# Optimization experiments

Measured on AMD Instinct MI355X. Metric: run time of the kernel, lower is better.

## Reference

```python
import jax, jax.numpy as jnp
import numpy as np

D, DFF, H, V, BS, NL, NG = 1024, 4096, 16, 32000, 128, 2, 2

def _ln(x, w, b, eps=1e-5):
    m = x.mean(-1, keepdims=True)
    v = ((x - m) ** 2).mean(-1, keepdims=True)
    return (x - m) / jnp.sqrt(v + eps) * w + b

def _full_attn(q, k, v):
    # q,k,v: [B,H,S,dk] ; manual max-subtract softmax with +1e-9 denom and clamp, per FullAttention
    dk = q.shape[-1]
    s = jnp.einsum('bhqd,bhkd->bhqk', q / jnp.sqrt(jnp.float32(dk)), k)
    s = s - s.max(-1, keepdims=True)
    e = jnp.exp(s)
    a = e / (e.sum(-1, keepdims=True) + 1e-9)
    a = jnp.clip(a, 1e-9, 1.0)
    return jnp.einsum('bhqk,bhkd->bhqd', a, v)

def _attn_layer(qi, ki, vi, lnw, lnb, pw, pb):
    # lnw/lnb: [4,D] (norm_q,k,v,out); pw: [4,D,D] (q,k,v,o, stored [in,out]); pb: [4,D]
    B, Sq, _ = qi.shape
    Sk = ki.shape[1]
    q = _ln(qi, lnw[0], lnb[0]) @ pw[0] + pb[0]
    k = _ln(ki, lnw[1], lnb[1]) @ pw[1] + pb[1]
    v = _ln(vi, lnw[2], lnb[2]) @ pw[2] + pb[2]
    dk = D // H
    q = q.reshape(B, Sq, H, dk).transpose(0, 2, 1, 3)
    k = k.reshape(B, Sk, H, dk).transpose(0, 2, 1, 3)
    v = v.reshape(B, Sk, H, dk).transpose(0, 2, 1, 3)
    o = _full_attn(q, k, v).transpose(0, 2, 1, 3).reshape(B, Sq, D)
    o = o @ pw[3] + pb[3]
    return _ln(o, lnw[3], lnb[3])

def _ffn(x, n1w, n1b, n2w, n2b, w1, b1, w2, b2):
    h = jax.nn.gelu(_ln(x, n1w, n1b) @ w1 + b1, approximate=False)
    return _ln(h @ w2 + b2 + x, n2w, n2b)

def _tlayer(x, lnw, lnb, pw, pb, w1, b1, w2, b2):
    # lnw/lnb: [6,D] (attn q,k,v,out norms, ffn norm1, ffn norm2)
    x = x + _attn_layer(x, x, x, lnw[:4], lnb[:4], pw, pb)
    return _ffn(x, lnw[4], lnb[4], lnw[5], lnb[5], w1, b1, w2, b2)

def _pe(S, d):
    pos = jnp.arange(S, dtype=jnp.float32)[:, None]
    div = jnp.exp(jnp.arange(0, d, 2, dtype=jnp.float32) * (-np.log(10000.0) / d))
    pe = jnp.zeros((S, d), jnp.float32)
    pe = pe.at[:, 0::2].set(jnp.sin(pos * div))
    pe = pe.at[:, 1::2].set(jnp.cos(pos * div))
    return pe

def setup_inputs() -> dict:
    key = jax.random.key(0)
    ks = iter(jax.random.split(key, 64))
    nrm = lambda shp: jax.random.normal(next(ks), shp, jnp.float32) * 0.02
    inp = {
        'x': jax.random.randint(next(ks), (4, 4096), 0, V, dtype=jnp.int32).astype(jnp.int64),
        'emb': nrm((V, D)),
        'in_ln_w': jnp.ones((D,)), 'in_ln_b': jnp.zeros((D,)),
        'loc_ln_w': jnp.ones((NL, 6, D)), 'loc_ln_b': jnp.zeros((NL, 6, D)),
        'loc_pw': nrm((NL, 4, D, D)), 'loc_pb': jnp.zeros((NL, 4, D)),
        'loc_w1': nrm((NL, D, DFF)), 'loc_b1': jnp.zeros((NL, DFF)),
        'loc_w2': nrm((NL, DFF, D)), 'loc_b2': jnp.zeros((NL, D)),
        'locn_w': jnp.ones((D,)), 'locn_b': jnp.zeros((D,)),
        'pool_q': nrm((1, 1, D)),
        'pool_n_w': jnp.ones((D,)), 'pool_n_b': jnp.zeros((D,)),
        'pool_ln_w': jnp.ones((4, D)), 'pool_ln_b': jnp.zeros((4, D)),
        'pool_pw': nrm((4, D, D)), 'pool_pb': jnp.zeros((4, D)),
        'glob_ln_w': jnp.ones((NG, 6, D)), 'glob_ln_b': jnp.zeros((NG, 6, D)),
        'glob_pw': nrm((NG, 4, D, D)), 'glob_pb': jnp.zeros((NG, 4, D)),
        'glob_w1': nrm((NG, D, DFF)), 'glob_b1': jnp.zeros((NG, DFF)),
        'glob_w2': nrm((NG, DFF, D)), 'glob_b2': jnp.zeros((NG, D)),
        'out_ln_w': jnp.ones((D,)), 'out_ln_b': jnp.zeros((D,)),
        'out_w': nrm((D, V)), 'out_b': jnp.zeros((V,)),
    }
    return inp

def reference(x, emb, in_ln_w, in_ln_b, loc_ln_w, loc_ln_b, loc_pw, loc_pb,
              loc_w1, loc_b1, loc_w2, loc_b2, locn_w, locn_b,
              pool_q, pool_n_w, pool_n_b, pool_ln_w, pool_ln_b, pool_pw, pool_pb,
              glob_ln_w, glob_ln_b, glob_pw, glob_pb, glob_w1, glob_b1, glob_w2, glob_b2,
              out_ln_w, out_ln_b, out_w, out_b):
    B, S = x.shape
    nb = S // BS
    h = jnp.clip(emb[x], -100.0, 100.0) + _pe(S, D)[None]
    h = _ln(h, in_ln_w, in_ln_b)
    h = h.reshape(B * nb, BS, D)  # local blocks
    for i in range(NL):
        h = jnp.clip(_tlayer(h, loc_ln_w[i], loc_ln_b[i], loc_pw[i], loc_pb[i],
                             loc_w1[i], loc_b1[i], loc_w2[i], loc_b2[i]), -100.0, 100.0)
    h = _ln(h, locn_w, locn_b)
    # attention pooling of each block to one vector
    hp = _ln(h, pool_n_w, pool_n_b)
    q = jnp.broadcast_to(pool_q, (B * nb, 1, D))
    g = _attn_layer(q, hp, hp, pool_ln_w, pool_ln_b, pool_pw, pool_pb)[:, 0].reshape(B, nb, D)
    for i in range(NG):
        g = jnp.clip(_tlayer(g, glob_ln_w[i], glob_ln_b[i], glob_pw[i], glob_pb[i],
                             glob_w1[i], glob_b1[i], glob_w2[i], glob_b2[i]), -100.0, 100.0)
    g = _ln(g, out_ln_w, out_ln_b)
    return g @ out_w + out_b  # [B, num_blocks, vocab]
```

## Files before the change

kernel.cpp:

```cpp
#include <hip/hip_runtime.h>
#include <hip/hip_bf16.h>
#include <math.h>

#define DEV __device__ __forceinline__

typedef __attribute__((ext_vector_type(8))) short bf16x8;
typedef __attribute__((ext_vector_type(4))) float f32x4;
typedef unsigned short u16;

constexpr int D_ = 1024, NTOK = 16384, SEQ = 4096;

DEV u16 f2b(float f){
  union{float f;unsigned u;} v; v.f=f;
  unsigned r = (v.u + 0x7fffu + ((v.u>>16)&1u))>>16;
  return (u16)r;
}
DEV float b2f(u16 h){ union{unsigned u;float f;} v; v.u=((unsigned)h)<<16; return v.f; }

DEV float gelu_f(float x){
  float z = 0.7978845608028654f*(x + 0.044715f*x*x*x);
  float e = __expf(-2.f*z);
  float t = 2.f/(1.f+e) - 1.f;
  return 0.5f*x*(1.f+t);
}

DEV void gld16(const void* g, void* l){
  __builtin_amdgcn_global_load_lds((const __attribute__((address_space(1))) void*)g,
                                   (__attribute__((address_space(3))) void*)l, 16, 0, 0);
}

#define BAR()    __builtin_amdgcn_s_barrier()
#define SCHED0() __builtin_amdgcn_sched_barrier(0)
#define LGKM0()  asm volatile("s_waitcnt lgkmcnt(0)" ::: "memory")
#define VM0()    asm volatile("s_waitcnt vmcnt(0)" ::: "memory")

DEV float blockSum(float v){
  __shared__ float sb[4];
  #pragma unroll
  for(int m=32;m>=1;m>>=1) v += __shfl_xor(v, m, 64);
  int lane = threadIdx.x & 63, wv = threadIdx.x >> 6;
  __syncthreads();
  if(lane==0) sb[wv]=v;
  __syncthreads();
  float r = sb[0]+sb[1]+sb[2]+sb[3];
  __syncthreads();
  return r;
}

__global__ __launch_bounds__(256) void detect_k(const int* __restrict__ xr, int* __restrict__ flag){
  int tid=threadIdx.x; float cnt=0.f;
  for(int i=tid;i<8192;i+=256) if(xr[2*i+1]!=0) cnt+=1.f;
  cnt = blockSum(cnt);
  if(tid==0) *flag = (cnt < 64.f) ? 1 : 0;
}

__global__ __launch_bounds__(256) void embed_k(const void* __restrict__ xv, const int* __restrict__ flag,
      const float* __restrict__ emb, const float* __restrict__ w, const float* __restrict__ b,
      u16* __restrict__ out, u16* __restrict__ outn){
  int t = blockIdx.x;
  int id;
  if(*flag) id = (int)((const long long*)xv)[t];
  else      id = ((const int*)xv)[t];
  int s = t & (SEQ-1);
  int d0 = threadIdx.x*4;
  float4 e4 = *(const float4*)(emb + (size_t)id*D_ + d0);
  float vv[4] = {e4.x, e4.y, e4.z, e4.w};
  float acc = 0.f;
  #pragma unroll
  for(int i=0;i<4;i++){
    float e = fminf(fmaxf(vv[i], -100.f), 100.f);
    int d = d0+i;
    float fr = expf(-(float)(d & ~1) * (9.210340371976184f/(float)D_));
    float ang = (float)s * fr;
    e += (d&1) ? cosf(ang) : sinf(ang);
    vv[i]=e; acc+=e;
  }
  float mean = blockSum(acc)*(1.f/D_);
  float var=0.f;
  #pragma unroll
  for(int i=0;i<4;i++){ float dd=vv[i]-mean; var+=dd*dd; }
  var = blockSum(var)*(1.f/D_);
  float rs = rsqrtf(var+1e-5f);
  float y[4];
  #pragma unroll
  for(int i=0;i<4;i++) y[i] = (vv[i]-mean)*rs*w[d0+i]+b[d0+i];
  ushort4 o; o.x=f2b(y[0]); o.y=f2b(y[1]); o.z=f2b(y[2]); o.w=f2b(y[3]);
  *(ushort4*)(out + (size_t)t*D_ + d0) = o;
  float m2 = blockSum(y[0]+y[1]+y[2]+y[3])*(1.f/D_);
  float v2=0.f;
  #pragma unroll
  for(int i=0;i<4;i++){ float dd=y[i]-m2; v2+=dd*dd; }
  v2 = blockSum(v2)*(1.f/D_);
  float rs2 = rsqrtf(v2+1e-5f);
  ushort4 on; on.x=f2b((y[0]-m2)*rs2); on.y=f2b((y[1]-m2)*rs2); on.z=f2b((y[2]-m2)*rs2); on.w=f2b((y[3]-m2)*rs2);
  *(ushort4*)(outn + (size_t)t*D_ + d0) = on;
}

template<int MODE,int WRN>
__global__ __launch_bounds__(256) void ln_k(const u16* __restrict__ in, const u16* __restrict__ res,
      const float* __restrict__ w, const float* __restrict__ b, u16* __restrict__ out,
      u16* __restrict__ outn){
  int t = blockIdx.x; int d0 = threadIdx.x*4;
  ushort4 r4 = *(const ushort4*)(in + (size_t)t*D_ + d0);
  float vv[4] = {b2f(r4.x),b2f(r4.y),b2f(r4.z),b2f(r4.w)};
  float mean = blockSum(vv[0]+vv[1]+vv[2]+vv[3])*(1.f/D_);
  float var=0.f;
  #pragma unroll
  for(int i=0;i<4;i++){ float dd=vv[i]-mean; var+=dd*dd; }
  var = blockSum(var)*(1.f/D_);
  float rs = rsqrtf(var+1e-5f);
  float rv[4]={0,0,0,0};
  if(MODE==3){
    ushort4 q4 = *(const ushort4*)(res + (size_t)t*D_ + d0);
    rv[0]=b2f(q4.x); rv[1]=b2f(q4.y); rv[2]=b2f(q4.z); rv[3]=b2f(q4.w);
  }
  float y[4];
  #pragma unroll
  for(int i=0;i<4;i++){
    float v = (vv[i]-mean)*rs;
    v = v*w[d0+i]+b[d0+i];
    if(MODE==2) v = fminf(fmaxf(v,-100.f),100.f);
    if(MODE==3) v += rv[i];
    y[i]=v;
  }
  ushort4 o; o.x=f2b(y[0]); o.y=f2b(y[1]); o.z=f2b(y[2]); o.w=f2b(y[3]);
  *(ushort4*)(out + (size_t)t*D_ + d0) = o;
  if(WRN){
    float m2 = blockSum(y[0]+y[1]+y[2]+y[3])*(1.f/D_);
    float v2=0.f;
    #pragma unroll
    for(int i=0;i<4;i++){ float dd=y[i]-m2; v2+=dd*dd; }
    v2 = blockSum(v2)*(1.f/D_);
    float rs2 = rsqrtf(v2+1e-5f);
    ushort4 on; on.x=f2b((y[0]-m2)*rs2); on.y=f2b((y[1]-m2)*rs2); on.z=f2b((y[2]-m2)*rs2); on.w=f2b((y[3]-m2)*rs2);
    *(ushort4*)(outn + (size_t)t*D_ + d0) = on;
  }
}

__global__ __launch_bounds__(256) void ln3x_k(const u16* __restrict__ in,
    const float* __restrict__ w1,const float* __restrict__ b1,
    const float* __restrict__ w2,const float* __restrict__ b2, u16* __restrict__ out){
  int t=blockIdx.x, d0=threadIdx.x*4;
  ushort4 r4 = *(const ushort4*)(in + (size_t)t*D_ + d0);
  float vv[4]={b2f(r4.x),b2f(r4.y),b2f(r4.z),b2f(r4.w)};
  #pragma unroll
  for(int pass=0;pass<3;pass++){
    float mean = blockSum(vv[0]+vv[1]+vv[2]+vv[3])*(1.f/D_);
    float var=0.f;
    #pragma unroll
    for(int i=0;i<4;i++){ float dd=vv[i]-mean; var+=dd*dd; }
    var = blockSum(var)*(1.f/D_);
    float rs = rsqrtf(var+1e-5f);
    #pragma unroll
    for(int i=0;i<4;i++){
      float y=(vv[i]-mean)*rs;
      if(pass==0) y = y*w1[d0+i]+b1[d0+i];
      else if(pass==1) y = y*w2[d0+i]+b2[d0+i];
      vv[i]=y;
    }
  }
  ushort4 o;
  o.x=f2b(vv[0]); o.y=f2b(vv[1]); o.z=f2b(vv[2]); o.w=f2b(vv[3]);
  *(ushort4*)(out + (size_t)t*D_ + d0) = o;
}

__global__ __launch_bounds__(256) void lnrow_k(const float* __restrict__ x, const float* __restrict__ w,
      const float* __restrict__ b, float* __restrict__ out){
  int d0=threadIdx.x*4;
  float vv[4]={x[d0],x[d0+1],x[d0+2],x[d0+3]};
  float mean = blockSum(vv[0]+vv[1]+vv[2]+vv[3])*(1.f/D_);
  float var=0.f;
  #pragma unroll
  for(int i=0;i<4;i++){ float dd=vv[i]-mean; var+=dd*dd; }
  var = blockSum(var)*(1.f/D_);
  float rs = rsqrtf(var+1e-5f);
  #pragma unroll
  for(int i=0;i<4;i++) out[d0+i]=(vv[i]-mean)*rs*w[d0+i]+b[d0+i];
}

#define TF_BODY(W, ldW, lnw, Wt, Kd, n0, k0)                                 \
  {                                                                          \
    int ty = threadIdx.x>>6, tx = threadIdx.x&63;                            \
    _Pragma("unroll")                                                        \
    for(int p=0;p<16;p++){                                                   \
      int row = p*4+ty;                                                      \
      float sc = (lnw) ? (lnw)[(k0)+row] : 1.f;                              \
      T[row][tx] = (W)[(size_t)((k0)+row)*(ldW) + (n0)+tx]*sc;               \
    }                                                                        \
    __syncthreads();                                                         \
    _Pragma("unroll")                                                        \
    for(int p=0;p<16;p++){                                                   \
      int row = p*4+ty;                                                      \
      (Wt)[(size_t)((n0)+row)*(Kd) + (k0)+tx] = f2b(T[tx][row]);             \
    }                                                                        \
  }

__global__ __launch_bounds__(256) void tf_k(const float* __restrict__ W, int ldW,
      const float* __restrict__ lnw, u16* __restrict__ Wt, int Kd){
  __shared__ float T[64][65];
  int n0 = blockIdx.x*64, k0 = blockIdx.y*64;
  TF_BODY(W, ldW, lnw, Wt, Kd, n0, k0)
}

__global__ __launch_bounds__(256) void prep_tf_layer_k(const float* __restrict__ pw,
      const float* __restrict__ w1, const float* __restrict__ w2, const float* __restrict__ lw,
      u16* __restrict__ Wqk, u16* __restrict__ Wv, u16* __restrict__ Wo,
      u16* __restrict__ W1t, u16* __restrict__ W2t){
  __shared__ float T[64][65];
  int bid = blockIdx.x;
  const float* W; int ldW; const float* lnw; u16* Wt; int Kd, n0, k0;
  if(bid < 1024){
    int m = bid>>8, t = bid&255;
    n0 = (t&15)*64; k0 = (t>>4)*64;
    W = pw + (size_t)m*1024*1024; ldW = 1024; Kd = 1024;
    lnw = (m<3) ? lw + m*1024 : nullptr;
    Wt = (m==0)?Wqk : (m==1)?(Wqk+1024*1024) : (m==2)?Wv : Wo;
  } else if(bid < 2048){
    int t = bid-1024;
    n0 = (t&63)*64; k0 = (t>>6)*64;
    W = w1; ldW = 4096; Kd = 1024; lnw = lw+4*1024; Wt = W1t;
  } else {
    int t = bid-2048;
    n0 = (t&15)*64; k0 = (t>>4)*64;
    W = w2; ldW = 1024; Kd = 4096; lnw = nullptr; Wt = W2t;
  }
  TF_BODY(W, ldW, lnw, Wt, Kd, n0, k0)
}

__global__ __launch_bounds__(256) void prep_tf_pool_k(const float* __restrict__ pw,
      const float* __restrict__ lw, u16* __restrict__ PWkv, u16* __restrict__ PWo){
  __shared__ float T[64][65];
  int bid = blockIdx.x;
  int m = 1 + (bid>>8), t = bid&255;
  int n0 = (t&15)*64, k0 = (t>>4)*64;
  const float* W = pw + (size_t)m*1024*1024;
  const float* lnw = (m<3) ? lw + m*1024 : nullptr;
  u16* Wt = (m==1)?PWkv : (m==2)?(PWkv+1024*1024) : PWo;
  TF_BODY(W, 1024, lnw, Wt, 1024, n0, k0)
}

DEV void bias_body(const float* W, int ldW, int Kd, const float* lnb, float pbv, float* out){
  int tid = threadIdx.x;
  float chk = 0.f;
  if(lnb){ for(int k=tid;k<Kd;k+=256) chk += fabsf(lnb[k]); }
  chk = blockSum(chk);
  if(chk==0.f){ if(tid==0) *out = pbv; return; }
  float s=0.f;
  for(int k=tid;k<Kd;k+=256) s += lnb[k]*W[(size_t)k*ldW];
  s = blockSum(s);
  if(tid==0) *out = pbv + s;
}

__global__ __launch_bounds__(256) void bias_k(const float* __restrict__ W, int ldW,
      const float* __restrict__ lnb, const float* __restrict__ pb, float* __restrict__ out, int Kd){
  int j = blockIdx.x;
  bias_body(W + j, ldW, Kd, lnb, pb[j], out + j);
}

__global__ __launch_bounds__(256) void prep_bias_layer_k(const float* __restrict__ pw,
      const float* __restrict__ w1, const float* __restrict__ w2,
      const float* __restrict__ lb, const float* __restrict__ pb,
      const float* __restrict__ b1in, const float* __restrict__ b2in,
      float* __restrict__ Bqk, float* __restrict__ Bv, float* __restrict__ Bo,
      float* __restrict__ B1, float* __restrict__ B2){
  int j = blockIdx.x;
  const float* W; int ldW, Kd; const float* lnb; float pbv; float* out;
  const size_t MM = 1024ull*1024;
  if(j<2048){ int m=j>>10; int col=j&1023; W=pw+m*MM+col; ldW=1024; Kd=1024; lnb=lb+m*1024; pbv=pb[m*1024+col]; out=Bqk+j; }
  else if(j<3072){ int col=j-2048; W=pw+2*MM+col; ldW=1024; Kd=1024; lnb=lb+2*1024; pbv=pb[2*1024+col]; out=Bv+col; }
  else if(j<4096){ int col=j-3072; W=pw+3*MM+col; ldW=1024; Kd=1024; lnb=nullptr; pbv=pb[3*1024+col]; out=Bo+col; }
  else if(j<8192){ int col=j-4096; W=w1+col; ldW=4096; Kd=1024; lnb=lb+4*1024; pbv=b1in[col]; out=B1+col; }
  else { int col=j-8192; W=w2+col; ldW=1024; Kd=4096; lnb=nullptr; pbv=b2in[col]; out=B2+col; }
  bias_body(W, ldW, Kd, lnb, pbv, out);
}

__global__ __launch_bounds__(256) void prep_bias_pool_k(const float* __restrict__ pw,
      const float* __restrict__ lb, const float* __restrict__ pb,
      float* __restrict__ Pbkv, float* __restrict__ Pbo){
  int j = blockIdx.x;
  const size_t MM = 1024ull*1024;
  int m = 1 + (j>>10), col = j&1023;
  const float* lnb = (m<3) ? lb + m*1024 : nullptr;
  float* out = (m==1)?(Pbkv+col) : (m==2)?(Pbkv+1024+col) : (Pbo+col);
  bias_body(pw + m*MM + col, 1024, 1024, lnb, pb[m*1024+col], out);
}

__global__ __launch_bounds__(256) void matvec_k(const float* __restrict__ xn, const float* __restrict__ W,
      int ldW, const float* __restrict__ bias, float* __restrict__ out){
  int j=blockIdx.x, tid=threadIdx.x;
  float s=0.f;
  for(int k=tid;k<1024;k+=256) s += xn[k]*W[(size_t)k*ldW + j];
  s=blockSum(s);
  if(tid==0) out[j]=s+bias[j];
}

template<int EPI,int OUTF,int TV>
__global__ __launch_bounds__(256) void gemm_k(const u16* __restrict__ A, const u16* __restrict__ Bt,
      const float* __restrict__ bias, const u16* __restrict__ resid, void* __restrict__ Cout,
      int M, int N, int K, int ldc){
  __shared__ u16 SH[32768];
  int tid = threadIdx.x, lane = tid&63, wv = tid>>6;
  int g = lane>>4, l15 = lane&15;
  int GX = gridDim.x, GY = gridDim.y;
  int nwg = GX*GY;
  int flat = blockIdx.y*GX + blockIdx.x;
  int q = nwg>>3, r = nwg&7, xcd = flat&7, idx = flat>>3;
  int f = (xcd<r ? xcd*(q+1) : r*(q+1)+(xcd-r)*q) + idx;
  int by, bx;
  if((GY & 7) == 0){
    int sbs = GX<<3;
    int s = f / sbs, rr2 = f - s*sbs;
    by = s*8 + (rr2 & 7);
    bx = rr2 >> 3;
  } else {
    by = f/GX; bx = f - by*GX;
  }
  int row0 = by*128, col0 = bx*128;
  int wr = wv>>1, wc = wv&1;
  int e0 = wv*512 + lane*8;
  f32x4 acc[4][4] = {};
  auto STAGE = [&](int buf, int t){
    u16* base = SH + buf*16384;
    int k0 = t<<6;
    #pragma unroll
    for(int c=0;c<4;c++){
      int e = c*2048 + e0;
      int row = e>>6;
      int slx = ((e>>3)&7) ^ (row&7);
      gld16(A  + (size_t)(row0 + row)*K + (k0 + slx*8), &base[e]);
      gld16(Bt + (size_t)(col0 + row)*K + (k0 + slx*8), &base[8192 + e]);
    }
  };
  int nt = K>>6;
  STAGE(0, 0);
  VM0(); BAR(); SCHED0();
  #pragma unroll 2
  for(int t=0;t<nt;t++){
    int b = t&1;
    if(t+1<nt) STAGE(b^1, t+1);
    bf16x8 a[2][4], bb[2][4];
    #pragma unroll
    for(int ks=0;ks<2;ks++){
      #pragma unroll
      for(int m=0;m<4;m++){
        int ra = wr*64+m*16+l15;
        a[ks][m] = *(const bf16x8*)&SH[b*16384 + ra*64 + (((ks*4+g) ^ (ra&7))<<3)];
      }
      #pragma unroll
      for(int n=0;n<4;n++){
        int rb = wc*64+n*16+l15;
        bb[ks][n] = *(const bf16x8*)&SH[b*16384 + 8192 + rb*64 + (((ks*4+g) ^ (rb&7))<<3)];
      }
    }
    #pragma unroll
    for(int ks=0;ks<2;ks++)
      #pragma unroll
      for(int m=0;m<4;m++)
        #pragma unroll
        for(int n=0;n<4;n++)
          acc[m][n] = __builtin_amdgcn_mfma_f32_16x16x32_bf16(a[ks][m], bb[ks][n], acc[m][n], 0,0,0);
    if(t+1<nt){
      VM0(); LGKM0(); BAR(); SCHED0();
    }
  }
  if(TV){
    __syncthreads();
    u16* Tb = SH;
    #pragma unroll
    for(int m=0;m<4;m++){
      #pragma unroll
      for(int n=0;n<4;n++){
        int c = wc*64 + n*16 + l15;
        float bs = bias[col0 + c];
        #pragma unroll
        for(int r2=0;r2<4;r2++){
          int Rl = wr*64 + m*16 + g*4 + r2;
          Tb[c*128 + (Rl ^ ((c&7)<<4))] = f2b(acc[m][n][r2]+bs);
        }
      }
    }
    __syncthreads();
    for(int p=tid*4; p<16384; p+=1024){
      int c = p>>7, rr = p&127;
      int rs = rr ^ ((c&7)<<4);
      ushort4 v4;
      v4.x = Tb[c*128+rs]; v4.y = Tb[c*128+rs+1]; v4.z = Tb[c*128+rs+2]; v4.w = Tb[c*128+rs+3];
      *(ushort4*)((u16*)Cout + (size_t)(col0+c)*M + row0 + rr) = v4;
    }
  } else {
    #pragma unroll
    for(int m=0;m<4;m++){
      #pragma unroll
      for(int n=0;n<4;n++){
        int Cc = col0 + wc*64 + n*16 + l15;
        float bs = bias[Cc];
        #pragma unroll
        for(int r2=0;r2<4;r2++){
          int R = row0 + wr*64 + m*16 + g*4 + r2;
          float v = acc[m][n][r2] + bs;
          if(EPI==1) v = gelu_f(v);
          if(EPI==2) v += b2f(resid[(size_t)R*ldc + Cc]);
          if(OUTF) ((float*)Cout)[(size_t)R*ldc + Cc] = v;
          else     ((u16*)Cout)[(size_t)R*ldc + Cc] = f2b(v);
        }
      }
    }
  }
}

__global__ __launch_bounds__(256) void attnl_k(const u16* __restrict__ QK, const u16* __restrict__ VT,
      u16* __restrict__ AT){
  __shared__ u16 SP[16384];
  __shared__ u16 Vt[8192];
  __shared__ float rmax[256], rsum[256];
  int tid=threadIdx.x, lane=tid&63, wv=tid>>6, g=lane>>4, l15=lane&15;
  int lb = blockIdx.x>>4, h = blockIdx.x&15;
  int wr=wv>>1, wc=wv&1;
  #pragma unroll
  for(int c=0;c<4;c++){
    int chunk = c*2048 + wv*512;
    int e = chunk + lane*8;
    int rq = e>>6;
    int sq = ((e>>3)&7) ^ (rq&7);
    int rv = e>>7;
    int sv = ((e>>3)&15) ^ (rv&15);
    gld16(QK + (size_t)(lb*128 + rq)*2048 + h*64 + sq*8,        &SP[chunk]);
    gld16(QK + (size_t)(lb*128 + rq)*2048 + 1024 + h*64 + sq*8, &SP[8192+chunk]);
    gld16(VT + (size_t)(h*64 + rv)*16384 + lb*128 + sv*8,       &Vt[chunk]);
  }
  __syncthreads();
  f32x4 s[4][4] = {};
  #pragma unroll
  for(int ks=0;ks<2;ks++){
    bf16x8 a[4], b[4];
    #pragma unroll
    for(int m=0;m<4;m++){
      int ra = wr*64+m*16+l15;
      a[m] = *(const bf16x8*)&SP[ra*64 + (((ks*4+g) ^ (ra&7))<<3)];
    }
    #pragma unroll
    for(int n=0;n<4;n++){
      int rb = wc*64+n*16+l15;
      b[n] = *(const bf16x8*)&SP[8192 + rb*64 + (((ks*4+g) ^ (rb&7))<<3)];
    }
    #pragma unroll
    for(int m=0;m<4;m++)
      #pragma unroll
      for(int n=0;n<4;n++)
        s[m][n] = __builtin_amdgcn_mfma_f32_16x16x32_bf16(a[m], b[n], s[m][n], 0,0,0);
  }
  #pragma unroll
  for(int m=0;m<4;m++)
    #pragma unroll
    for(int n=0;n<4;n++) s[m][n] *= 0.125f;
  #pragma unroll
  for(int m=0;m<4;m++)
    #pragma unroll
    for(int r=0;r<4;r++){
      float mx = fmaxf(fmaxf(s[m][0][r],s[m][1][r]),fmaxf(s[m][2][r],s[m][3][r]));
      #pragma unroll
      for(int msk=1;msk<16;msk<<=1) mx = fmaxf(mx, __shfl_xor(mx,msk,64));
      if(l15==0) rmax[(wr*64+m*16+g*4+r)*2+wc]=mx;
    }
  __syncthreads();
  #pragma unroll
  for(int m=0;m<4;m++)
    #pragma unroll
    for(int r=0;r<4;r++){
      int row = wr*64+m*16+g*4+r;
      float M2 = fmaxf(rmax[row*2], rmax[row*2+1]);
      float sm=0.f;
      #pragma unroll
      for(int n=0;n<4;n++){ float e = expf(s[m][n][r]-M2); s[m][n][r]=e; sm+=e; }
      #pragma unroll
      for(int msk=1;msk<16;msk<<=1) sm += __shfl_xor(sm,msk,64);
      if(l15==0) rsum[row*2+wc]=sm;
    }
  __syncthreads();
  #pragma unroll
  for(int m=0;m<4;m++)
    #pragma unroll
    for(int r=0;r<4;r++){
      int row = wr*64+m*16+g*4+r;
      float den = rsum[row*2]+rsum[row*2+1]+1e-9f;
      #pragma unroll
      for(int n=0;n<4;n++){
        float a = s[m][n][r]/den;
        a = fminf(fmaxf(a,1e-9f),1.f);
        int col = wc*64+n*16+l15;
        SP[row*128 + ((((col>>3) ^ (row&15))<<3) | (col&7))] = f2b(a);
      }
    }
  __syncthreads();
  f32x4 o[4][2] = {};
  #pragma unroll
  for(int ks=0;ks<4;ks++){
    bf16x8 a[4], b[2];
    #pragma unroll
    for(int m=0;m<4;m++){
      int ra = wr*64+m*16+l15;
      a[m] = *(const bf16x8*)&SP[ra*128 + (((ks*4+g) ^ (ra&15))<<3)];
    }
    #pragma unroll
    for(int n=0;n<2;n++){
      int rv = wc*32+n*16+l15;
      b[n] = *(const bf16x8*)&Vt[rv*128 + (((ks*4+g) ^ (rv&15))<<3)];
    }
    #pragma unroll
    for(int m=0;m<4;m++)
      #pragma unroll
      for(int n=0;n<2;n++)
        o[m][n] = __builtin_amdgcn_mfma_f32_16x16x32_bf16(a[m], b[n], o[m][n], 0,0,0);
  }
  #pragma unroll
  for(int m=0;m<4;m++)
    #pragma unroll
    for(int n=0;n<2;n++)
      #pragma unroll
      for(int r=0;r<4;r++)
        AT[(size_t)(lb*128 + wr*64+m*16+g*4+r)*1024 + h*64 + wc*32+n*16+l15] = f2b(o[m][n][r]);
}

__global__ __launch_bounds__(256) void poolattn_k(const float* __restrict__ qp, const u16* __restrict__ KV,
      u16* __restrict__ g0){
  int lb = blockIdx.x, tid = threadIdx.x;
  __shared__ float sc[16*128];
  for(int p=tid;p<2048;p+=256){
    int h=p>>7, j=p&127;
    const u16* krow = KV + (size_t)(lb*128+j)*2048 + h*64;
    float s=0.f;
    for(int d=0;d<64;d++) s += qp[h*64+d]*b2f(krow[d]);
    sc[h*128+j] = s*0.125f;
  }
  __syncthreads();
  if(tid<16){
    float* r=&sc[tid*128];
    float mx=r[0];
    for(int j=1;j<128;j++) mx=fmaxf(mx,r[j]);
    float sm=0.f;
    for(int j=0;j<128;j++){ float e=expf(r[j]-mx); r[j]=e; sm+=e; }
    sm+=1e-9f;
    for(int j=0;j<128;j++) r[j]=fminf(fmaxf(r[j]/sm,1e-9f),1.f);
  }
  __syncthreads();
  for(int c=tid;c<1024;c+=256){
    int h=c>>6;
    float acc=0.f;
    for(int j=0;j<128;j++) acc += sc[h*128+j]*b2f(KV[(size_t)(lb*128+j)*2048 + 1024 + c]);
    g0[(size_t)lb*1024 + c] = f2b(acc);
  }
}

__global__ __launch_bounds__(256) void attng_k(const u16* __restrict__ QKV, u16* __restrict__ OUT){
  int bb = blockIdx.x>>4, h = blockIdx.x&15;
  __shared__ float sc[32*32];
  int tid=threadIdx.x;
  for(int p=tid;p<1024;p+=256){
    int i=p>>5, j=p&31;
    const u16* q = QKV + (size_t)(bb*32+i)*3072 + h*64;
    const u16* k = QKV + (size_t)(bb*32+j)*3072 + 1024 + h*64;
    float s=0.f;
    for(int d=0;d<64;d++) s += b2f(q[d])*b2f(k[d]);
    sc[p] = s*0.125f;
  }
  __syncthreads();
  if(tid<32){
    float* r=&sc[tid*32];
    float mx=r[0];
    for(int j=1;j<32;j++) mx=fmaxf(mx,r[j]);
    float sm=0.f;
    for(int j=0;j<32;j++){ float e=expf(r[j]-mx); r[j]=e; sm+=e; }
    sm+=1e-9f;
    for(int j=0;j<32;j++) r[j]=fminf(fmaxf(r[j]/sm,1e-9f),1.f);
  }
  __syncthreads();
  for(int p=tid;p<2048;p+=256){
    int i=p>>6, d=p&63;
    float acc=0.f;
    for(int j=0;j<32;j++) acc += sc[i*32+j]*b2f(QKV[(size_t)(bb*32+j)*3072 + 2048 + h*64 + d]);
    OUT[(size_t)(bb*32+i)*1024 + h*64 + d] = f2b(acc);
  }
}

extern "C" void kernel_launch(void* const* d_in, const int* in_sizes, int n_in,
                              void* d_out, int out_size, void* d_ws, size_t ws_size,
                              hipStream_t stream) {
  (void)in_sizes; (void)n_in; (void)out_size;
  const void*  x       = d_in[0];
  const float* emb     = (const float*)d_in[1];
  const float* in_ln_w = (const float*)d_in[2];
  const float* in_ln_b = (const float*)d_in[3];
  const float* loc_ln_w= (const float*)d_in[4];
  const float* loc_ln_b= (const float*)d_in[5];
  const float* loc_pw  = (const float*)d_in[6];
  const float* loc_pb  = (const float*)d_in[7];
  const float* loc_w1  = (const float*)d_in[8];
  const float* loc_b1  = (const float*)d_in[9];
  const float* loc_w2  = (const float*)d_in[10];
  const float* loc_b2  = (const float*)d_in[11];
  const float* locn_w  = (const float*)d_in[12];
  const float* locn_b  = (const float*)d_in[13];
  const float* pool_q  = (const float*)d_in[14];
  const float* pool_n_w= (const float*)d_in[15];
  const float* pool_n_b= (const float*)d_in[16];
  const float* pool_ln_w=(const float*)d_in[17];
  const float* pool_ln_b=(const float*)d_in[18];
  const float* pool_pw = (const float*)d_in[19];
  const float* pool_pb = (const float*)d_in[20];
  const float* glob_ln_w=(const float*)d_in[21];
  const float* glob_ln_b=(const float*)d_in[22];
  const float* glob_pw = (const float*)d_in[23];
  const float* glob_pb = (const float*)d_in[24];
  const float* glob_w1 = (const float*)d_in[25];
  const float* glob_b1 = (const float*)d_in[26];
  const float* glob_w2 = (const float*)d_in[27];
  const float* glob_b2 = (const float*)d_in[28];
  const float* out_ln_w= (const float*)d_in[29];
  const float* out_ln_b= (const float*)d_in[30];
  const float* out_w   = (const float*)d_in[31];
  const float* out_b   = (const float*)d_in[32];

  char* wsb = (char*)d_ws;
  size_t off = 0;
  auto AL = [&](size_t n)->char*{ size_t o=(off+255)&~(size_t)255; off=o+n; return wsb+o; };

  int*  flag = (int*)AL(256);
  u16*  WA   = (u16*)AL(12ull*1024*1024*2);
  float* BA  = (float*)AL(12*1024*4);
  float* qn  = (float*)AL(1024*4);
  float* qp  = (float*)AL(1024*4);
  float* Hb  = (float*)AL(32000*4);
  u16*  R    = (u16*)AL(64ull*1024*1024*2);
  u16*  X    = (u16*)AL((size_t)NTOK*1024*2);
  u16*  XN   = (u16*)AL((size_t)NTOK*1024*2);
  u16*  G    = (u16*)AL(128ull*1024*2);
  u16*  GN   = (u16*)AL(128ull*1024*2);
  u16*  GQKV = (u16*)AL(128ull*3072*2);
  u16*  GAT  = (u16*)AL(128ull*1024*2);
  u16*  GO   = (u16*)AL(128ull*1024*2);
  u16*  GFH  = (u16*)AL(128ull*4096*2);
  u16*  g0   = (u16*)AL(128ull*1024*2);
  if(off > ws_size) return;

  u16 *LWqk = WA, *LWv = WA+2097152, *LWo = WA+3145728, *LW1 = WA+4194304, *LW2 = WA+8388608;
  float *Lbqk = BA, *Lbv = BA+2048, *Lbo = BA+3072, *Lb1 = BA+4096, *Lb2 = BA+8192;
  u16 *GWqkv = WA, *GWo = WA+3145728, *GW1 = WA+4194304, *GW2 = WA+8388608;
  float *Gbqkv = BA, *Gbo = BA+3072, *Gb1 = BA+4096, *Gb2 = BA+8192;
  u16 *PWkv = WA, *PWo = WA+2097152;
  float *Pbkv = BA, *Pbo = BA+2048;
  u16 *QKb = R, *VTb = R+33554432, *ATb = R+50331648;
  u16 *FH  = R;
  u16 *KVb = R;
  u16 *HW  = R;
  u16 *Ob  = XN;

  const size_t MM = 1024ull*1024;

  detect_k<<<1,256,0,stream>>>((const int*)x, flag);
  embed_k<<<NTOK,256,0,stream>>>(x, flag, emb, in_ln_w, in_ln_b, X, XN);

  for(int l=0;l<2;l++){
    const float* pw = loc_pw + (size_t)l*4*MM;
    const float* lw = loc_ln_w + (size_t)l*6*1024;
    const float* lb = loc_ln_b + (size_t)l*6*1024;
    const float* pb = loc_pb + (size_t)l*4*1024;
    const float* w1 = loc_w1 + (size_t)l*1024*4096;
    const float* w2 = loc_w2 + (size_t)l*4096*1024;
    prep_tf_layer_k<<<3072,256,0,stream>>>(pw, w1, w2, lw, LWqk, LWv, LWo, LW1, LW2);
    prep_bias_layer_k<<<9216,256,0,stream>>>(pw, w1, w2, lb, pb,
        loc_b1+(size_t)l*4096, loc_b2+(size_t)l*1024, Lbqk, Lbv, Lbo, Lb1, Lb2);

    gemm_k<0,0,0><<<dim3(16,128),256,0,stream>>>(XN, LWqk, Lbqk, nullptr, QKb, NTOK, 2048, 1024, 2048);
    gemm_k<0,0,1><<<dim3(8,128),256,0,stream>>>(XN, LWv, Lbv, nullptr, VTb, NTOK, 1024, 1024, 0);
    attnl_k<<<128*16,256,0,stream>>>(QKb, VTb, ATb);
    gemm_k<0,0,0><<<dim3(8,128),256,0,stream>>>(ATb, LWo, Lbo, nullptr, Ob, NTOK, 1024, 1024, 1024);
    ln_k<3,1><<<NTOK,256,0,stream>>>(Ob, X, lw+3*1024, lb+3*1024, X, XN);
    gemm_k<1,0,0><<<dim3(32,128),256,0,stream>>>(XN, LW1, Lb1, nullptr, FH, NTOK, 4096, 1024, 4096);
    gemm_k<2,0,0><<<dim3(8,128),256,0,stream>>>(FH, LW2, Lb2, X, Ob, NTOK, 1024, 4096, 1024);
    ln_k<2,1><<<NTOK,256,0,stream>>>(Ob, nullptr, lw+5*1024, lb+5*1024, X, XN);
  }

  prep_tf_pool_k<<<768,256,0,stream>>>(pool_pw, pool_ln_w, PWkv, PWo);
  prep_bias_pool_k<<<3072,256,0,stream>>>(pool_pw, pool_ln_b, pool_pb, Pbkv, Pbo);
  lnrow_k<<<1,256,0,stream>>>(pool_q, pool_ln_w, pool_ln_b, qn);
  matvec_k<<<1024,256,0,stream>>>(qn, pool_pw, 1024, pool_pb, qp);
  ln3x_k<<<NTOK,256,0,stream>>>(X, locn_w, locn_b, pool_n_w, pool_n_b, XN);
  gemm_k<0,0,0><<<dim3(16,128),256,0,stream>>>(XN, PWkv, Pbkv, nullptr, KVb, NTOK, 2048, 1024, 2048);
  poolattn_k<<<128,256,0,stream>>>(qp, KVb, g0);
  gemm_k<0,0,0><<<dim3(8,1),256,0,stream>>>(g0, PWo, Pbo, nullptr, GO, 128, 1024, 1024, 1024);
  ln_k<1,1><<<128,256,0,stream>>>(GO, nullptr, pool_ln_w+3*1024, pool_ln_b+3*1024, G, GN);

  for(int l=0;l<2;l++){
    const float* pw = glob_pw + (size_t)l*4*MM;
    const float* lw = glob_ln_w + (size_t)l*6*1024;
    const float* lb = glob_ln_b + (size_t)l*6*1024;
    const float* pb = glob_pb + (size_t)l*4*1024;
    const float* w1 = glob_w1 + (size_t)l*1024*4096;
    const float* w2 = glob_w2 + (size_t)l*4096*1024;
    prep_tf_layer_k<<<3072,256,0,stream>>>(pw, w1, w2, lw, GWqkv, GWqkv+2097152, GWo, GW1, GW2);
    prep_bias_layer_k<<<9216,256,0,stream>>>(pw, w1, w2, lb, pb,
        glob_b1+(size_t)l*4096, glob_b2+(size_t)l*1024, Gbqkv, Gbqkv+2048, Gbo, Gb1, Gb2);

    gemm_k<0,0,0><<<dim3(24,1),256,0,stream>>>(GN, GWqkv, Gbqkv, nullptr, GQKV, 128, 3072, 1024, 3072);
    attng_k<<<64,256,0,stream>>>(GQKV, GAT);
    gemm_k<0,0,0><<<dim3(8,1),256,0,stream>>>(GAT, GWo, Gbo, nullptr, GO, 128, 1024, 1024, 1024);
    ln_k<3,1><<<128,256,0,stream>>>(GO, G, lw+3*1024, lb+3*1024, G, GN);
    gemm_k<1,0,0><<<dim3(32,1),256,0,stream>>>(GN, GW1, Gb1, nullptr, GFH, 128, 4096, 1024, 4096);
    gemm_k<2,0,0><<<dim3(8,1),256,0,stream>>>(GFH, GW2, Gb2, G, GO, 128, 1024, 4096, 1024);
    ln_k<2,1><<<128,256,0,stream>>>(GO, nullptr, lw+5*1024, lb+5*1024, G, GN);
  }

  tf_k<<<dim3(500,16),256,0,stream>>>(out_w, 32000, out_ln_w, HW, 1024);
  bias_k<<<32000,256,0,stream>>>(out_w, 32000, out_ln_b, out_b, Hb, 1024);
  gemm_k<0,1,0><<<dim3(250,1),256,0,stream>>>(GN, HW, Hb, nullptr, d_out, 128, 32000, 1024, 32000);
}
```

Baseline: 1.915 ms.

## Add 256x256-tile 8-wave bf16 GEMM kernel for large token GEMMs

Introduces a 512-thread GEMM kernel with 256x256 output tiles, XOR-swizzled LDS staging through global_load_lds, and double buffering where the next K tile is prefetched while MFMA quadrants run. It also remaps workgroups across XCDs for better L2 locality. All large local-layer and pooling GEMMs switch to it. The larger tiles cut global/L2 traffic per FLOP, at the cost of one workgroup per CU, 128KB of dynamic LDS and heavy register use.

```diff
diff --git a/kernel.cpp b/kernel.cpp
--- a/kernel.cpp
+++ b/kernel.cpp
@@ -32,6 +32,7 @@
 #define BAR()    __builtin_amdgcn_s_barrier()
 #define SCHED0() __builtin_amdgcn_sched_barrier(0)
 #define LGKM0()  asm volatile("s_waitcnt lgkmcnt(0)" ::: "memory")
+#define VM8()    asm volatile("s_waitcnt vmcnt(8)" ::: "memory")
 #define VM0()    asm volatile("s_waitcnt vmcnt(0)" ::: "memory")
 
 DEV float blockSum(float v){
@@ -402,6 +403,138 @@
           if(EPI==2) v += b2f(resid[(size_t)R*ldc + Cc]);
           if(OUTF) ((float*)Cout)[(size_t)R*ldc + Cc] = v;
           else     ((u16*)Cout)[(size_t)R*ldc + Cc] = f2b(v);
+        }
+      }
+    }
+  }
+}
+
+template<int EPI,int TV>
+__global__ __launch_bounds__(512,1) void gemm256_k(const u16* __restrict__ A, const u16* __restrict__ Bt,
+      const float* __restrict__ bias, const u16* __restrict__ resid, void* __restrict__ Cout,
+      int M, int N, int K, int ldc){
+  extern __shared__ u16 LS[];
+  int tid = threadIdx.x, lane = tid&63, wid = tid>>6;
+  int g = lane>>4, l15 = lane&15;
+  int wm = wid>>2, wn = wid&3;
+  int GX = gridDim.x, GY = gridDim.y, nwg = GX*GY;
+  int flat = blockIdx.y*GX + blockIdx.x;
+  int q = nwg>>3, r = nwg&7, xcd = flat&7, idx = flat>>3;
+  int f = (xcd<r ? xcd*(q+1) : r*(q+1)+(xcd-r)*q) + idx;
+  int by, bx;
+  if((GY&7)==0){ int sbs = GX<<3; int s = f/sbs, rr2 = f - s*sbs; by = s*8 + (rr2&7); bx = rr2>>3; }
+  else { by = f/GX; bx = f - by*GX; }
+  int row0 = by*256, col0 = bx*256;
+
+  f32x4 acc[8][4] = {};
+  bf16x8 areg[2][4], breg[2][4];
+
+  auto STAGE_A = [&](int b, int t){
+    #pragma unroll
+    for(int j=0;j<4;j++){
+      int e = j*4096 + tid*8;
+      int row = e>>6;
+      int slx = ((e>>3)&7) ^ (row&7);
+      gld16(A + (size_t)(row0 + row)*K + (t<<6) + slx*8, &LS[b*16384 + e]);
+    }
+  };
+  auto STAGE_B = [&](int b, int t){
+    #pragma unroll
+    for(int j=0;j<4;j++){
+      int e = j*4096 + tid*8;
+      int row = e>>6;
+      int slx = ((e>>3)&7) ^ (row&7);
+      gld16(Bt + (size_t)(col0 + row)*K + (t<<6) + slx*8, &LS[32768 + b*16384 + e]);
+    }
+  };
+  auto READ_A = [&](int b, int mh){
+    #pragma unroll
+    for(int ks=0;ks<2;ks++)
+      #pragma unroll
+      for(int m=0;m<4;m++){
+        int rih = mh*64 + m*16 + l15;
+        areg[ks][m] = *(const bf16x8*)&LS[b*16384 + wm*8192 + rih*64 + (((ks*4+g)^(rih&7))<<3)];
+      }
+  };
+  auto READ_B = [&](int b, int nh){
+    #pragma unroll
+    for(int ks=0;ks<2;ks++)
+      #pragma unroll
+      for(int n=0;n<2;n++){
+        int rih = (wn&1)*64 + (nh*2+n)*16 + l15;
+        breg[ks][nh*2+n] = *(const bf16x8*)&LS[32768 + b*16384 + (wn>>1)*8192 + rih*64 + (((ks*4+g)^(rih&7))<<3)];
+      }
+  };
+  auto MFMA_Q = [&](int mh, int nh){
+    __builtin_amdgcn_s_setprio(1);
+    #pragma unroll
+    for(int ks=0;ks<2;ks++)
+      #pragma unroll
+      for(int m=0;m<4;m++)
+        #pragma unroll
+        for(int n=0;n<2;n++)
+          acc[mh*4+m][nh*2+n] = __builtin_amdgcn_mfma_f32_16x16x32_bf16(
+              areg[ks][m], breg[ks][nh*2+n], acc[mh*4+m][nh*2+n], 0,0,0);
+    __builtin_amdgcn_s_setprio(0);
+  };
+
+  int NT = K>>6;
+  STAGE_B(0,0); STAGE_A(0,0);
+  STAGE_B(1,1); STAGE_A(1,1);
+  VM8(); SCHED0(); BAR();
+
+  for(int t=0;t<NT;t++){
+    int b = t&1;
+    bool st = (t+2<NT);
+    READ_B(b,0); READ_A(b,0);
+    BAR(); LGKM0(); SCHED0(); MFMA_Q(0,0); BAR();
+    READ_B(b,1);
+    BAR(); LGKM0(); SCHED0(); MFMA_Q(0,1); BAR();
+    READ_A(b,1);
+    if(st) STAGE_B(b, t+2);
+    BAR(); LGKM0(); SCHED0(); MFMA_Q(1,0); BAR();
+    if(st) STAGE_A(b, t+2);
+    if(st){ VM8(); } else { VM0(); }
+    SCHED0(); BAR(); MFMA_Q(1,1); BAR();
+  }
+
+  if(TV){
+    __syncthreads();
+    #pragma unroll
+    for(int mi=0;mi<8;mi++){
+      #pragma unroll
+      for(int n=0;n<4;n++){
+        int c = wn*64 + n*16 + l15;
+        float bs = bias[col0 + c];
+        #pragma unroll
+        for(int r2=0;r2<4;r2++){
+          int Rl = wm*128 + mi*16 + g*4 + r2;
+          LS[c*256 + (Rl ^ ((c&15)<<4))] = f2b(acc[mi][n][r2]+bs);
+        }
+      }
+    }
+    __syncthreads();
+    for(int p=tid*4; p<65536; p+=2048){
+      int c = p>>8, rr = p&255;
+      int rs = rr ^ ((c&15)<<4);
+      ushort4 v4;
+      v4.x = LS[c*256+rs]; v4.y = LS[c*256+rs+1]; v4.z = LS[c*256+rs+2]; v4.w = LS[c*256+rs+3];
+      *(ushort4*)((u16*)Cout + (size_t)(col0+c)*M + row0 + rr) = v4;
+    }
+  } else {
+    #pragma unroll
+    for(int mi=0;mi<8;mi++){
+      #pragma unroll
+      for(int n=0;n<4;n++){
+        int Cc = col0 + wn*64 + n*16 + l15;
+        float bs = bias[Cc];
+        #pragma unroll
+        for(int r2=0;r2<4;r2++){
+          int R = row0 + wm*128 + mi*16 + g*4 + r2;
+          float v = acc[mi][n][r2] + bs;
+          if(EPI==1) v = gelu_f(v);
+          if(EPI==2) v += b2f(resid[(size_t)R*ldc + Cc]);
+          ((u16*)Cout)[(size_t)R*ldc + Cc] = f2b(v);
         }
       }
     }
@@ -655,6 +788,7 @@
   u16 *Ob  = XN;
 
   const size_t MM = 1024ull*1024;
+  const size_t SM256 = 131072;
 
   detect_k<<<1,256,0,stream>>>((const int*)x, flag);
   embed_k<<<NTOK,256,0,stream>>>(x, flag, emb, in_ln_w, in_ln_b, X, XN);
@@ -670,13 +804,13 @@
     prep_bias_layer_k<<<9216,256,0,stream>>>(pw, w1, w2, lb, pb,
         loc_b1+(size_t)l*4096, loc_b2+(size_t)l*1024, Lbqk, Lbv, Lbo, Lb1, Lb2);
 
-    gemm_k<0,0,0><<<dim3(16,128),256,0,stream>>>(XN, LWqk, Lbqk, nullptr, QKb, NTOK, 2048, 1024, 2048);
-    gemm_k<0,0,1><<<dim3(8,128),256,0,stream>>>(XN, LWv, Lbv, nullptr, VTb, NTOK, 1024, 1024, 0);
+    gemm256_k<0,0><<<dim3(8,64),512,SM256,stream>>>(XN, LWqk, Lbqk, nullptr, QKb, NTOK, 2048, 1024, 2048);
+    gemm256_k<0,1><<<dim3(4,64),512,SM256,stream>>>(XN, LWv, Lbv, nullptr, VTb, NTOK, 1024, 1024, 0);
     attnl_k<<<128*16,256,0,stream>>>(QKb, VTb, ATb);
-    gemm_k<0,0,0><<<dim3(8,128),256,0,stream>>>(ATb, LWo, Lbo, nullptr, Ob, NTOK, 1024, 1024, 1024);
+    gemm256_k<0,0><<<dim3(4,64),512,SM256,stream>>>(ATb, LWo, Lbo, nullptr, Ob, NTOK, 1024, 1024, 1024);
     ln_k<3,1><<<NTOK,256,0,stream>>>(Ob, X, lw+3*1024, lb+3*1024, X, XN);
-    gemm_k<1,0,0><<<dim3(32,128),256,0,stream>>>(XN, LW1, Lb1, nullptr, FH, NTOK, 4096, 1024, 4096);
-    gemm_k<2,0,0><<<dim3(8,128),256,0,stream>>>(FH, LW2, Lb2, X, Ob, NTOK, 1024, 4096, 1024);
+    gemm256_k<1,0><<<dim3(16,64),512,SM256,stream>>>(XN, LW1, Lb1, nullptr, FH, NTOK, 4096, 1024, 4096);
+    gemm256_k<2,0><<<dim3(4,64),512,SM256,stream>>>(FH, LW2, Lb2, X, Ob, NTOK, 1024, 4096, 1024);
     ln_k<2,1><<<NTOK,256,0,stream>>>(Ob, nullptr, lw+5*1024, lb+5*1024, X, XN);
   }
 
@@ -685,7 +819,7 @@
   lnrow_k<<<1,256,0,stream>>>(pool_q, pool_ln_w, pool_ln_b, qn);
   matvec_k<<<1024,256,0,stream>>>(qn, pool_pw, 1024, pool_pb, qp);
   ln3x_k<<<NTOK,256,0,stream>>>(X, locn_w, locn_b, pool_n_w, pool_n_b, XN);
-  gemm_k<0,0,0><<<dim3(16,128),256,0,stream>>>(XN, PWkv, Pbkv, nullptr, KVb, NTOK, 2048, 1024, 2048);
+  gemm256_k<0,0><<<dim3(8,64),512,SM256,stream>>>(XN, PWkv, Pbkv, nullptr, KVb, NTOK, 2048, 1024, 2048);
   poolattn_k<<<128,256,0,stream>>>(qp, KVb, g0);
   gemm_k<0,0,0><<<dim3(8,1),256,0,stream>>>(g0, PWo, Pbo, nullptr, GO, 128, 1024, 1024, 1024);
   ln_k<1,1><<<128,256,0,stream>>>(GO, nullptr, pool_ln_w+3*1024, pool_ln_b+3*1024, G, GN);
```

Result: slower. 2.124 ms (+10.9%).
